# Kernel tuning notes

Measured on AMD Instinct MI355X. Metric: run time of the kernel, lower is better.

Reference implementation:

```python
import jax, jax.numpy as jnp
import numpy as np

N_NODES = 100000
N_EDGES = 1600000
D_IN = 128
D_OUT = 128


def setup_inputs() -> dict:
    key = jax.random.key(0)
    ks = jax.random.split(key, 7)
    stdv = 1.0 / np.sqrt(D_OUT)
    x = jax.random.normal(ks[0], (N_NODES, D_IN), dtype=jnp.float32)
    W = jax.random.normal(ks[1], (D_IN, D_OUT), dtype=jnp.float32) * stdv
    lin_bias = jax.random.uniform(ks[2], (D_OUT,), minval=-stdv, maxval=stdv, dtype=jnp.float32)
    bias = jax.random.uniform(ks[3], (D_OUT,), minval=-stdv, maxval=stdv, dtype=jnp.float32)
    adj_rows = jax.random.randint(ks[4], (N_EDGES,), 0, N_NODES, dtype=jnp.int32)
    adj_cols = jax.random.randint(ks[5], (N_EDGES,), 0, N_NODES, dtype=jnp.int32)
    adj_vals = jax.random.uniform(ks[6], (N_EDGES,), dtype=jnp.float32)
    return {"x": x, "W": W, "lin_bias": lin_bias, "bias": bias,
            "adj_rows": adj_rows, "adj_cols": adj_cols, "adj_vals": adj_vals}


def reference(x, W, lin_bias, bias, adj_rows, adj_cols, adj_vals):
    # support = Linear(x)  -> [N, D_OUT]
    support = x @ W + lin_bias
    # out = spmm(adj, support): out[r] = sum_e vals[e] * support[cols[e]] for rows[e]==r
    msgs = adj_vals[:, None] * support[adj_cols]            # [E, D_OUT]
    out = jax.ops.segment_sum(msgs, adj_rows, num_segments=N_NODES)
    return out + bias
```

## Files before the change

### kernel.cpp

```cpp
#include <hip/hip_runtime.h>
#include <hip/hip_bf16.h>

#define N_NODES 100000
#define N_EDGES 1600000
#define D 128

#define NBLK 512
#define EPB (N_EDGES / NBLK)
#define BROWS 128
#define NB 782
#define PCAP 2816

typedef __attribute__((ext_vector_type(8))) short short8;
typedef __attribute__((ext_vector_type(4))) float f32x4;

__device__ inline unsigned short f2bf(float f) {
  union { float f; unsigned u; } c; c.f = f;
  const unsigned u = c.u;
  return (unsigned short)((u + 0x7FFF + ((u >> 16) & 1)) >> 16);
}
__device__ inline float bflo(unsigned u) { return __int_as_float(u << 16); }
__device__ inline float bfhi(unsigned u) { return __int_as_float(u & 0xFFFF0000u); }

__global__ __launch_bounds__(256) void prep_kernel(
    const float* __restrict__ W, unsigned short* __restrict__ Wt,
    int* __restrict__ gcur) {
  const int b = blockIdx.x;
  if (b < 16) {
    const int t = b * 256 + threadIdx.x;
    const int k = t >> 5, n4 = (t & 31) * 4;
    const float4 w = *(const float4*)(W + k * D + n4);
    Wt[(n4 + 0) * D + k] = f2bf(w.x);
    Wt[(n4 + 1) * D + k] = f2bf(w.y);
    Wt[(n4 + 2) * D + k] = f2bf(w.z);
    Wt[(n4 + 3) * D + k] = f2bf(w.w);
  } else {
    for (int i = threadIdx.x; i < NB; i += 256) gcur[i] = 0;
  }
}

#define GR 128
#define LDK 136
__global__ __launch_bounds__(512) void fused_kernel(
    const float* __restrict__ x, const unsigned short* __restrict__ Wt,
    const float* __restrict__ lin_bias, unsigned short* __restrict__ support,
    const int* __restrict__ rows, const int* __restrict__ cols,
    const float* __restrict__ vals, int* __restrict__ gcur,
    unsigned* __restrict__ pairs, unsigned char* __restrict__ rowlo) {
  __shared__ __align__(16) char smem[GR * LDK * 2];

  const int t = threadIdx.x;
  const int w = t >> 6, lane = t & 63;

  if (blockIdx.x < NBLK) {
    int* cnt = (int*)smem;
    int* cur = cnt + NB;
    int* gbase = cur + NB;
    unsigned* spa = (unsigned*)(gbase + NB);
    unsigned* srow = spa + EPB;
    int* wsum = (int*)(srow + EPB);
    const int blk = blockIdx.x;
    const int base = blk * EPB;

    for (int i = t; i < NB; i += 512) cnt[i] = 0;
    __syncthreads();
    for (int i = t; i < EPB; i += 512)
      atomicAdd(&cnt[rows[base + i] >> 7], 1);
    __syncthreads();

    int s2[2]; int ssum = 0;
#pragma unroll
    for (int j = 0; j < 2; ++j) {
      const int idx = t * 2 + j;
      s2[j] = (idx < NB) ? cnt[idx] : 0;
      ssum += s2[j];
    }
    int xi = ssum;
#pragma unroll
    for (int d = 1; d < 64; d <<= 1) {
      const int y = __shfl_up(xi, d, 64);
      if (lane >= d) xi += y;
    }
    if (lane == 63) wsum[w] = xi;
    __syncthreads();
    int pre = 0;
#pragma unroll
    for (int i = 0; i < 8; ++i) pre += (i < w) ? wsum[i] : 0;
    int ex = pre + xi - ssum;
#pragma unroll
    for (int j = 0; j < 2; ++j) {
      const int idx = t * 2 + j;
      if (idx < NB) cur[idx] = ex;
      ex += s2[j];
    }
    __syncthreads();

    for (int b = t; b < NB; b += 512) {
      const int c = cnt[b];
      gbase[b] = c ? atomicAdd(&gcur[b], c) : 0;
    }
    __syncthreads();

    for (int i = t; i < EPB; i += 512) {
      const int e = base + i;
      const int r = rows[e];
      const int b = r >> 7;
      const unsigned q = (unsigned)(vals[e] * 32767.f + 0.5f);
      const unsigned pr = ((unsigned)cols[e] << 15) | q;
      const int p = atomicAdd(&cur[b], 1);
      spa[p] = pr;
      srow[p] = (unsigned)r;
    }
    __syncthreads();

    for (int p = t; p < EPB; p += 512) {
      const unsigned r = srow[p];
      const int b = r >> 7;
      const int dst = gbase[b] + (p - (cur[b] - cnt[b]));
      if (dst < PCAP) {
        pairs[(size_t)b * PCAP + dst] = spa[p];
        rowlo[(size_t)b * PCAP + dst] = (unsigned char)(r & (BROWS - 1));
      }
    }
    return;
  }

  unsigned short* xb = (unsigned short*)smem;
  const int row0 = (blockIdx.x - NBLK) * GR;

  for (int i = t; i < GR * 32; i += 512) {
    const int r = i >> 5, k4 = (i & 31) * 4;
    const int row = row0 + r;
    float4 v = make_float4(0.f, 0.f, 0.f, 0.f);
    if (row < N_NODES) v = *(const float4*)(x + (size_t)row * D + k4);
    unsigned short* p = &xb[r * LDK + k4];
    p[0] = f2bf(v.x); p[1] = f2bf(v.y); p[2] = f2bf(v.z); p[3] = f2bf(v.w);
  }
  __syncthreads();

  const int m16 = lane & 15;
  const int quad = lane >> 4;

  f32x4 acc[8];
#pragma unroll
  for (int ct = 0; ct < 8; ++ct) acc[ct] = (f32x4){0.f, 0.f, 0.f, 0.f};

#pragma unroll
  for (int kc = 0; kc < 4; ++kc) {
    const int kof = kc * 32 + quad * 8;
    short8 a0 = *(const short8*)&xb[(w * 16 + m16) * LDK + kof];
#pragma unroll
    for (int ct = 0; ct < 8; ++ct) {
      const short8 b = *(const short8*)&Wt[(size_t)(ct * 16 + m16) * D + kof];
      acc[ct] = __builtin_amdgcn_mfma_f32_16x16x32_bf16(a0, b, acc[ct], 0, 0, 0);
    }
  }

#pragma unroll
  for (int ct = 0; ct < 8; ++ct) {
    const int col = ct * 16 + m16;
    const float lb = lin_bias[col];
    const int rbase = row0 + w * 16 + quad * 4;
#pragma unroll
    for (int i = 0; i < 4; ++i) {
      const int row = rbase + i;
      if (row < N_NODES)
        support[(size_t)row * D + col] = f2bf(acc[ct][i] + lb);
    }
  }
}

__global__ __launch_bounds__(512) void gather3_kernel(
    const int* __restrict__ gcur, const unsigned* __restrict__ pairs,
    const unsigned char* __restrict__ rowlo, const uint4* __restrict__ support,
    const float* __restrict__ bias, float* __restrict__ out) {
  __shared__ unsigned spair[PCAP];
  __shared__ unsigned char srl[PCAP];
  __shared__ unsigned short sidx[PCAP];
  __shared__ int rcnt[BROWS];
  __shared__ int rs[BROWS];
  __shared__ int rpos[BROWS];
  const int b = blockIdx.x, t = threadIdx.x;
  const int w = t >> 6, lane = t & 63;
  const int g = lane >> 4;
  const int c16 = lane & 15;
  const int r0 = b * BROWS;
  int m = gcur[b];
  if (m > PCAP) m = PCAP;
  const size_t pbase = (size_t)b * PCAP;

  for (int i = t; i < m; i += 512) {
    spair[i] = pairs[pbase + i];
    srl[i] = rowlo[pbase + i];
  }
  if (t < BROWS) rcnt[t] = 0;
  __syncthreads();
  for (int i = t; i < m; i += 512) atomicAdd(&rcnt[srl[i]], 1);
  __syncthreads();
  if (t < BROWS) rs[t] = rcnt[t];
  __syncthreads();
#pragma unroll
  for (int d = 1; d < BROWS; d <<= 1) {
    int v = 0;
    if (t < BROWS && t >= d) v = rs[t - d];
    __syncthreads();
    if (t < BROWS) rs[t] += v;
    __syncthreads();
  }
  if (t < BROWS) rpos[t] = rs[t] - rcnt[t];
  __syncthreads();
  for (int i = t; i < m; i += 512) {
    const int p = atomicAdd(&rpos[srl[i]], 1);
    sidx[p] = (unsigned short)i;
  }
  __syncthreads();

  for (int j = 0; j < 16; ++j) {
    const int rl = w * 16 + j;
    const int row = r0 + rl;
    if (row >= N_NODES) break;
    const int c = rcnt[rl];
    const int s = rs[rl] - c;

    float acc[8];
#pragma unroll
    for (int i = 0; i < 8; ++i) acc[i] = 0.f;

    for (int it = 0; it < c; it += 16) {
      const int ia = it + g;
      const int ib = it + 4 + g;
      const int ic = it + 8 + g;
      const int id = it + 12 + g;
      if (ia < c) {
        const unsigned p = spair[sidx[s + ia]];
        const float v = (float)(p & 0x7FFFu) * (1.f / 32767.f);
        const uint4 sv = support[(size_t)(p >> 15) * 16 + c16];
        acc[0] += v * bflo(sv.x); acc[1] += v * bfhi(sv.x);
        acc[2] += v * bflo(sv.y); acc[3] += v * bfhi(sv.y);
        acc[4] += v * bflo(sv.z); acc[5] += v * bfhi(sv.z);
        acc[6] += v * bflo(sv.w); acc[7] += v * bfhi(sv.w);
      }
      if (ib < c) {
        const unsigned p = spair[sidx[s + ib]];
        const float v = (float)(p & 0x7FFFu) * (1.f / 32767.f);
        const uint4 sv = support[(size_t)(p >> 15) * 16 + c16];
        acc[0] += v * bflo(sv.x); acc[1] += v * bfhi(sv.x);
        acc[2] += v * bflo(sv.y); acc[3] += v * bfhi(sv.y);
        acc[4] += v * bflo(sv.z); acc[5] += v * bfhi(sv.z);
        acc[6] += v * bflo(sv.w); acc[7] += v * bfhi(sv.w);
      }
      if (ic < c) {
        const unsigned p = spair[sidx[s + ic]];
        const float v = (float)(p & 0x7FFFu) * (1.f / 32767.f);
        const uint4 sv = support[(size_t)(p >> 15) * 16 + c16];
        acc[0] += v * bflo(sv.x); acc[1] += v * bfhi(sv.x);
        acc[2] += v * bflo(sv.y); acc[3] += v * bfhi(sv.y);
        acc[4] += v * bflo(sv.z); acc[5] += v * bfhi(sv.z);
        acc[6] += v * bflo(sv.w); acc[7] += v * bfhi(sv.w);
      }
      if (id < c) {
        const unsigned p = spair[sidx[s + id]];
        const float v = (float)(p & 0x7FFFu) * (1.f / 32767.f);
        const uint4 sv = support[(size_t)(p >> 15) * 16 + c16];
        acc[0] += v * bflo(sv.x); acc[1] += v * bfhi(sv.x);
        acc[2] += v * bflo(sv.y); acc[3] += v * bfhi(sv.y);
        acc[4] += v * bflo(sv.z); acc[5] += v * bfhi(sv.z);
        acc[6] += v * bflo(sv.w); acc[7] += v * bfhi(sv.w);
      }
    }

#pragma unroll
    for (int i = 0; i < 8; ++i) {
      acc[i] += __shfl_xor(acc[i], 16, 64);
      acc[i] += __shfl_xor(acc[i], 32, 64);
    }

    if (g == 0) {
      const float4 b0 = ((const float4*)bias)[c16 * 2 + 0];
      const float4 b1 = ((const float4*)bias)[c16 * 2 + 1];
      float4 o0, o1;
      o0.x = acc[0] + b0.x; o0.y = acc[1] + b0.y;
      o0.z = acc[2] + b0.z; o0.w = acc[3] + b0.w;
      o1.x = acc[4] + b1.x; o1.y = acc[5] + b1.y;
      o1.z = acc[6] + b1.z; o1.w = acc[7] + b1.w;
      float* op = out + (size_t)row * D + c16 * 8;
      *(float4*)(op + 0) = o0;
      *(float4*)(op + 4) = o1;
    }
  }
}

__global__ __launch_bounds__(256) void gemm_kernel(
    const float* __restrict__ x, const unsigned short* __restrict__ Wt,
    const float* __restrict__ lin_bias, unsigned short* __restrict__ support) {
  __shared__ unsigned short xb[GR * LDK];
  const int t = threadIdx.x;
  const int row0 = blockIdx.x * GR;

  for (int i = t; i < GR * 32; i += 256) {
    const int r = i >> 5, k4 = (i & 31) * 4;
    const int row = row0 + r;
    float4 v = make_float4(0.f, 0.f, 0.f, 0.f);
    if (row < N_NODES) v = *(const float4*)(x + (size_t)row * D + k4);
    unsigned short* p = &xb[r * LDK + k4];
    p[0] = f2bf(v.x); p[1] = f2bf(v.y); p[2] = f2bf(v.z); p[3] = f2bf(v.w);
  }
  __syncthreads();

  const int w = t >> 6;
  const int lane = t & 63;
  const int m16 = lane & 15;
  const int quad = lane >> 4;

  f32x4 acc[2][8];
#pragma unroll
  for (int rt = 0; rt < 2; ++rt)
#pragma unroll
    for (int ct = 0; ct < 8; ++ct) acc[rt][ct] = (f32x4){0.f, 0.f, 0.f, 0.f};

#pragma unroll
  for (int kc = 0; kc < 4; ++kc) {
    const int kof = kc * 32 + quad * 8;
    short8 a0 = *(const short8*)&xb[(w * 32 + 0 * 16 + m16) * LDK + kof];
    short8 a1 = *(const short8*)&xb[(w * 32 + 1 * 16 + m16) * LDK + kof];
#pragma unroll
    for (int ct = 0; ct < 8; ++ct) {
      const short8 b = *(const short8*)&Wt[(size_t)(ct * 16 + m16) * D + kof];
      acc[0][ct] = __builtin_amdgcn_mfma_f32_16x16x32_bf16(a0, b, acc[0][ct], 0, 0, 0);
      acc[1][ct] = __builtin_amdgcn_mfma_f32_16x16x32_bf16(a1, b, acc[1][ct], 0, 0, 0);
    }
  }

#pragma unroll
  for (int ct = 0; ct < 8; ++ct) {
    const int col = ct * 16 + m16;
    const float lb = lin_bias[col];
#pragma unroll
    for (int rt = 0; rt < 2; ++rt) {
      const int rbase = row0 + w * 32 + rt * 16 + quad * 4;
#pragma unroll
      for (int i = 0; i < 4; ++i) {
        const int row = rbase + i;
        if (row < N_NODES)
          support[(size_t)row * D + col] = f2bf(acc[rt][ct][i] + lb);
      }
    }
  }
}

__global__ __launch_bounds__(256) void init_out_kernel(
    const float* __restrict__ bias, float* __restrict__ out) {
  const size_t idx = (size_t)blockIdx.x * 256 + threadIdx.x;
  const float4 b = ((const float4*)bias)[idx & 31];
  ((float4*)out)[idx] = b;
}

__global__ __launch_bounds__(256) void scatter_kernel(
    const int* __restrict__ rows, const int* __restrict__ cols,
    const float* __restrict__ vals, const uint2* __restrict__ support,
    float* __restrict__ out) {
  const size_t tid = (size_t)blockIdx.x * 256 + threadIdx.x;
  const int e = (int)(tid >> 5);
  const int q = (int)(tid & 31);
  const int r = rows[e];
  const int c = cols[e];
  const float v = vals[e];
  const uint2 s = support[(size_t)c * 32 + q];
  float* o = out + (size_t)r * D + 4 * q;
  atomicAdd(o + 0, v * bflo(s.x));
  atomicAdd(o + 1, v * bfhi(s.x));
  atomicAdd(o + 2, v * bflo(s.y));
  atomicAdd(o + 3, v * bfhi(s.y));
}

extern "C" void kernel_launch(void* const* d_in, const int* in_sizes, int n_in,
                              void* d_out, int out_size, void* d_ws, size_t ws_size,
                              hipStream_t stream) {
  const float* x        = (const float*)d_in[0];
  const float* W        = (const float*)d_in[1];
  const float* lin_bias = (const float*)d_in[2];
  const float* bias     = (const float*)d_in[3];
  const int*   adj_rows = (const int*)d_in[4];
  const int*   adj_cols = (const int*)d_in[5];
  const float* adj_vals = (const float*)d_in[6];
  float* out = (float*)d_out;

  char* wsb = (char*)d_ws;
  unsigned short* support = (unsigned short*)wsb;
  unsigned*       pairs   = (unsigned*)(wsb + 25600000);
  unsigned char*  rowlo   = (unsigned char*)(wsb + 34408448);
  int*            gcur    = (int*)(wsb + 36610560);
  const size_t ws_needed = 36646464;

  const bool csr_path = (ws_size >= ws_needed);
  unsigned short* wt = (unsigned short*)(csr_path ? (wsb + 36613696)
                                                  : (wsb + 25600000));
  int* gcur_f = csr_path ? gcur : (int*)(wsb + 25600000 + 32768);

  prep_kernel<<<17, 256, 0, stream>>>(W, wt, gcur_f);

  if (csr_path) {
    fused_kernel<<<NBLK + (N_NODES + GR - 1) / GR, 512, 0, stream>>>(
        x, wt, lin_bias, support, adj_rows, adj_cols, adj_vals,
        gcur, pairs, rowlo);
    gather3_kernel<<<NB, 512, 0, stream>>>(gcur, pairs, rowlo,
                                           (const uint4*)support, bias, out);
  } else {
    gemm_kernel<<<(N_NODES + GR - 1) / GR, 256, 0, stream>>>(
        x, wt, lin_bias, support);
    init_out_kernel<<<12500, 256, 0, stream>>>(bias, out);
    scatter_kernel<<<200000, 256, 0, stream>>>(adj_rows, adj_cols, adj_vals,
                                               (const uint2*)support, out);
  }
}
```

Baseline: 240.8 us.

## Replace global atomic bucket scatter with per-block sorted runs and offset table

Each edge-partition block now writes its locally bucket-sorted edges contiguously along with a per-bucket run-start table, instead of reserving global slots through atomics on a shared bucket counter and scattering to bucket-major storage. The gather kernel has all 512 threads each read one partition's run for its bucket, prefix-scan the run lengths, and copy the runs into shared memory. This removes the global atomics, the counter zeroing in prep, and the scattered global writes. In exchange the gather reads are short, strided per-thread runs, which may coalesce poorly.

```diff
diff --git a/kernel.cpp b/kernel.cpp
--- a/kernel.cpp
+++ b/kernel.cpp
@@ -9,6 +9,7 @@
 #define EPB (N_EDGES / NBLK)
 #define BROWS 128
 #define NB 782
+#define NRS (NB + 1)
 #define PCAP 2816
 
 typedef __attribute__((ext_vector_type(8))) short short8;
@@ -23,20 +24,14 @@
 __device__ inline float bfhi(unsigned u) { return __int_as_float(u & 0xFFFF0000u); }
 
 __global__ __launch_bounds__(256) void prep_kernel(
-    const float* __restrict__ W, unsigned short* __restrict__ Wt,
-    int* __restrict__ gcur) {
-  const int b = blockIdx.x;
-  if (b < 16) {
-    const int t = b * 256 + threadIdx.x;
-    const int k = t >> 5, n4 = (t & 31) * 4;
-    const float4 w = *(const float4*)(W + k * D + n4);
-    Wt[(n4 + 0) * D + k] = f2bf(w.x);
-    Wt[(n4 + 1) * D + k] = f2bf(w.y);
-    Wt[(n4 + 2) * D + k] = f2bf(w.z);
-    Wt[(n4 + 3) * D + k] = f2bf(w.w);
-  } else {
-    for (int i = threadIdx.x; i < NB; i += 256) gcur[i] = 0;
-  }
+    const float* __restrict__ W, unsigned short* __restrict__ Wt) {
+  const int t = blockIdx.x * 256 + threadIdx.x;
+  const int k = t >> 5, n4 = (t & 31) * 4;
+  const float4 w = *(const float4*)(W + k * D + n4);
+  Wt[(n4 + 0) * D + k] = f2bf(w.x);
+  Wt[(n4 + 1) * D + k] = f2bf(w.y);
+  Wt[(n4 + 2) * D + k] = f2bf(w.z);
+  Wt[(n4 + 3) * D + k] = f2bf(w.w);
 }
 
 #define GR 128
@@ -45,8 +40,8 @@
     const float* __restrict__ x, const unsigned short* __restrict__ Wt,
     const float* __restrict__ lin_bias, unsigned short* __restrict__ support,
     const int* __restrict__ rows, const int* __restrict__ cols,
-    const float* __restrict__ vals, int* __restrict__ gcur,
-    unsigned* __restrict__ pairs, unsigned char* __restrict__ rowlo) {
+    const float* __restrict__ vals, unsigned* __restrict__ psort,
+    unsigned char* __restrict__ rsort, int* __restrict__ runstart) {
   __shared__ __align__(16) char smem[GR * LDK * 2];
 
   const int t = threadIdx.x;
@@ -55,10 +50,9 @@
   if (blockIdx.x < NBLK) {
     int* cnt = (int*)smem;
     int* cur = cnt + NB;
-    int* gbase = cur + NB;
-    unsigned* spa = (unsigned*)(gbase + NB);
-    unsigned* srow = spa + EPB;
-    int* wsum = (int*)(srow + EPB);
+    unsigned* spa = (unsigned*)(cur + NB);
+    unsigned char* srl = (unsigned char*)(spa + EPB);
+    int* wsum = (int*)(srl + EPB + 3);
     const int blk = blockIdx.x;
     const int base = blk * EPB;
 
@@ -90,15 +84,13 @@
 #pragma unroll
     for (int j = 0; j < 2; ++j) {
       const int idx = t * 2 + j;
-      if (idx < NB) cur[idx] = ex;
+      if (idx < NB) {
+        cur[idx] = ex;
+        runstart[(size_t)blk * NRS + idx] = ex;
+      }
       ex += s2[j];
     }
-    __syncthreads();
-
-    for (int b = t; b < NB; b += 512) {
-      const int c = cnt[b];
-      gbase[b] = c ? atomicAdd(&gcur[b], c) : 0;
-    }
+    if (t == 511) runstart[(size_t)blk * NRS + NB] = EPB;
     __syncthreads();
 
     for (int i = t; i < EPB; i += 512) {
@@ -109,18 +101,13 @@
       const unsigned pr = ((unsigned)cols[e] << 15) | q;
       const int p = atomicAdd(&cur[b], 1);
       spa[p] = pr;
-      srow[p] = (unsigned)r;
+      srl[p] = (unsigned char)(r & (BROWS - 1));
     }
     __syncthreads();
 
     for (int p = t; p < EPB; p += 512) {
-      const unsigned r = srow[p];
-      const int b = r >> 7;
-      const int dst = gbase[b] + (p - (cur[b] - cnt[b]));
-      if (dst < PCAP) {
-        pairs[(size_t)b * PCAP + dst] = spa[p];
-        rowlo[(size_t)b * PCAP + dst] = (unsigned char)(r & (BROWS - 1));
-      }
+      psort[(size_t)blk * EPB + p] = spa[p];
+      rsort[(size_t)blk * EPB + p] = srl[p];
     }
     return;
   }
@@ -171,12 +158,14 @@
 }
 
 __global__ __launch_bounds__(512) void gather3_kernel(
-    const int* __restrict__ gcur, const unsigned* __restrict__ pairs,
-    const unsigned char* __restrict__ rowlo, const uint4* __restrict__ support,
+    const int* __restrict__ runstart, const unsigned* __restrict__ psort,
+    const unsigned char* __restrict__ rsort, const uint4* __restrict__ support,
     const float* __restrict__ bias, float* __restrict__ out) {
   __shared__ unsigned spair[PCAP];
-  __shared__ unsigned char srl[PCAP];
+  __shared__ unsigned char srl2[PCAP];
   __shared__ unsigned short sidx[PCAP];
+  __shared__ int wsum8[8];
+  __shared__ int mtot_s;
   __shared__ int rcnt[BROWS];
   __shared__ int rs[BROWS];
   __shared__ int rpos[BROWS];
@@ -185,17 +174,36 @@
   const int g = lane >> 4;
   const int c16 = lane & 15;
   const int r0 = b * BROWS;
-  int m = gcur[b];
-  if (m > PCAP) m = PCAP;
-  const size_t pbase = (size_t)b * PCAP;
-
-  for (int i = t; i < m; i += 512) {
-    spair[i] = pairs[pbase + i];
-    srl[i] = rowlo[pbase + i];
-  }
+
+  const int rs0 = runstart[(size_t)t * NRS + b];
+  const int rl = runstart[(size_t)t * NRS + b + 1] - rs0;
+  int xi = rl;
+#pragma unroll
+  for (int d = 1; d < 64; d <<= 1) {
+    const int y = __shfl_up(xi, d, 64);
+    if (lane >= d) xi += y;
+  }
+  if (lane == 63) wsum8[w] = xi;
+  __syncthreads();
+  int pre = 0;
+#pragma unroll
+  for (int i = 0; i < 8; ++i) pre += (i < w) ? wsum8[i] : 0;
+  const int off = pre + xi - rl;
+  if (t == 511) mtot_s = off + rl;
   if (t < BROWS) rcnt[t] = 0;
   __syncthreads();
-  for (int i = t; i < m; i += 512) atomicAdd(&rcnt[srl[i]], 1);
+  const int m = min(mtot_s, PCAP);
+  const size_t sbase = (size_t)t * EPB + rs0;
+  for (int k = 0; k < rl; ++k) {
+    const int dst = off + k;
+    if (dst < PCAP) {
+      spair[dst] = psort[sbase + k];
+      srl2[dst] = rsort[sbase + k];
+    }
+  }
+  __syncthreads();
+
+  for (int i = t; i < m; i += 512) atomicAdd(&rcnt[srl2[i]], 1);
   __syncthreads();
   if (t < BROWS) rs[t] = rcnt[t];
   __syncthreads();
@@ -210,17 +218,17 @@
   if (t < BROWS) rpos[t] = rs[t] - rcnt[t];
   __syncthreads();
   for (int i = t; i < m; i += 512) {
-    const int p = atomicAdd(&rpos[srl[i]], 1);
+    const int p = atomicAdd(&rpos[srl2[i]], 1);
     sidx[p] = (unsigned short)i;
   }
   __syncthreads();
 
   for (int j = 0; j < 16; ++j) {
-    const int rl = w * 16 + j;
-    const int row = r0 + rl;
+    const int rl2 = w * 16 + j;
+    const int row = r0 + rl2;
     if (row >= N_NODES) break;
-    const int c = rcnt[rl];
-    const int s = rs[rl] - c;
+    const int c = rcnt[rl2];
+    const int s = rs[rl2] - c;
 
     float acc[8];
 #pragma unroll
@@ -386,24 +394,23 @@
   float* out = (float*)d_out;
 
   char* wsb = (char*)d_ws;
-  unsigned short* support = (unsigned short*)wsb;
-  unsigned*       pairs   = (unsigned*)(wsb + 25600000);
-  unsigned char*  rowlo   = (unsigned char*)(wsb + 34408448);
-  int*            gcur    = (int*)(wsb + 36610560);
-  const size_t ws_needed = 36646464;
+  unsigned short* support  = (unsigned short*)wsb;
+  unsigned*       psort    = (unsigned*)(wsb + 25600000);
+  unsigned char*  rsort    = (unsigned char*)(wsb + 32000000);
+  int*            runstart = (int*)(wsb + 33600000);
+  const size_t ws_needed = 35236352;
 
   const bool csr_path = (ws_size >= ws_needed);
-  unsigned short* wt = (unsigned short*)(csr_path ? (wsb + 36613696)
+  unsigned short* wt = (unsigned short*)(csr_path ? (wsb + 35203584)
                                                   : (wsb + 25600000));
-  int* gcur_f = csr_path ? gcur : (int*)(wsb + 25600000 + 32768);
-
-  prep_kernel<<<17, 256, 0, stream>>>(W, wt, gcur_f);
+
+  prep_kernel<<<16, 256, 0, stream>>>(W, wt);
 
   if (csr_path) {
     fused_kernel<<<NBLK + (N_NODES + GR - 1) / GR, 512, 0, stream>>>(
         x, wt, lin_bias, support, adj_rows, adj_cols, adj_vals,
-        gcur, pairs, rowlo);
-    gather3_kernel<<<NB, 512, 0, stream>>>(gcur, pairs, rowlo,
+        psort, rsort, runstart);
+    gather3_kernel<<<NB, 512, 0, stream>>>(runstart, psort, rsort,
                                            (const uint4*)support, bias, out);
   } else {
     gemm_kernel<<<(N_NODES + GR - 1) / GR, 256, 0, stream>>>(
```

New measurement: 247.4 us. 2.7% more time.
